# Kernel optimization log

Measured on AMD Instinct MI355X. Metric: run time of the kernel, lower is better.

Reference implementation:

```python
import jax, jax.numpy as jnp
import numpy as np

N = 50000   # nodes
E = 800000  # edges
D = 128     # input = hidden = output dim
G = 64      # graphs in batch


def setup_inputs() -> dict:
    key = jax.random.key(0)
    ks = jax.random.split(key, 12)
    s = 1.0 / np.sqrt(D)
    x = jax.random.normal(ks[0], (N, D), dtype=jnp.float32)
    edge_index = jax.random.randint(ks[1], (2, E), 0, N, dtype=jnp.int64)
    batch = jnp.sort(jax.random.randint(ks[2], (N,), 0, G, dtype=jnp.int64))
    return {
        "x": x,
        "W1": jax.random.normal(ks[3], (D, D), jnp.float32) * s,
        "b1": jnp.zeros((D,), jnp.float32),
        "W2": jax.random.normal(ks[4], (D, D), jnp.float32) * s,
        "b2": jnp.zeros((D,), jnp.float32),
        "W3": jax.random.normal(ks[5], (D, D), jnp.float32) * s,
        "b3": jnp.zeros((D,), jnp.float32),
        "Wm1": jax.random.normal(ks[6], (D, D), jnp.float32) * s,
        "bm1": jnp.zeros((D,), jnp.float32),
        "Wm2": jax.random.normal(ks[7], (D, D), jnp.float32) * s,
        "bm2": jnp.zeros((D,), jnp.float32),
        "edge_index": edge_index,
        "batch": batch,
    }


def _gcn_conv(x, W, b, src, dst, deg_isqrt, num_nodes):
    # PyG GCNConv: h = D^{-1/2}(A+I)D^{-1/2} X W + b  (self-loops included in src/dst)
    h = x @ W  # [N, Dout]
    norm = deg_isqrt[src] * deg_isqrt[dst]  # [E+N]
    msg = h[src] * norm[:, None]            # gather + scale
    out = jax.ops.segment_sum(msg, dst, num_segments=num_nodes)  # scatter-add
    return out + b


def reference(x, W1, b1, W2, b2, W3, b3, Wm1, bm1, Wm2, bm2, edge_index, batch):
    num_nodes = x.shape[0]
    loop = jnp.arange(num_nodes, dtype=edge_index.dtype)
    src = jnp.concatenate([edge_index[0], loop])  # add self-loops
    dst = jnp.concatenate([edge_index[1], loop])
    # degree with self-loops (edge_weight = 1), computed on target nodes
    deg = jax.ops.segment_sum(jnp.ones_like(dst, dtype=x.dtype), dst,
                              num_segments=num_nodes)
    deg_isqrt = jnp.where(deg > 0, jax.lax.rsqrt(deg), 0.0)

    h = jax.nn.relu(_gcn_conv(x, W1, b1, src, dst, deg_isqrt, num_nodes))
    h = jax.nn.relu(_gcn_conv(h, W2, b2, src, dst, deg_isqrt, num_nodes))
    h = _gcn_conv(h, W3, b3, src, dst, deg_isqrt, num_nodes)

    # global_mean_pool over graph ids
    sums = jax.ops.segment_sum(h, batch, num_segments=G)
    cnts = jax.ops.segment_sum(jnp.ones((num_nodes,), h.dtype), batch,
                               num_segments=G)
    pooled = sums / jnp.maximum(cnts, 1.0)[:, None]  # [G, D]

    out = jax.nn.relu(pooled @ Wm1 + bm1) @ Wm2 + bm2
    return out
```

## Files before the change

kernel.cpp:

```cpp
#include <hip/hip_runtime.h>
#include <hip/hip_bf16.h>

typedef __attribute__((ext_vector_type(8))) short short8;
typedef __attribute__((ext_vector_type(4))) float floatx4;

#define SLAB_CAP 96

static __device__ __forceinline__ ushort f2b(float f) {
    __hip_bfloat16 h = __float2bfloat16(f);
    return __builtin_bit_cast(ushort, h);
}
static __device__ __forceinline__ float blo(uint u) {
    return __builtin_bit_cast(float, u << 16);
}
static __device__ __forceinline__ float bhi(uint u) {
    return __builtin_bit_cast(float, u & 0xffff0000u);
}
static __device__ __forceinline__ float b2f(ushort u) {
    return __builtin_bit_cast(float, (uint)u << 16);
}
static __device__ __forceinline__ uint pack2(float lo, float hi) {
    return (uint)f2b(lo) | ((uint)f2b(hi) << 16);
}

static __device__ __forceinline__ void fill_body(int bid, const int* __restrict__ src,
                                                 const int* __restrict__ dst, int E,
                                                 int* __restrict__ deg_cnt,
                                                 int* __restrict__ slab) {
    int e0 = (bid * 256 + threadIdx.x) * 4;
    if (e0 + 3 < E) {
        int4 s = *(const int4*)(src + e0);
        int4 d = *(const int4*)(dst + e0);
        int p0 = atomicAdd(&deg_cnt[d.x], 1);
        int p1 = atomicAdd(&deg_cnt[d.y], 1);
        int p2 = atomicAdd(&deg_cnt[d.z], 1);
        int p3 = atomicAdd(&deg_cnt[d.w], 1);
        if (p0 < SLAB_CAP) slab[d.x * SLAB_CAP + p0] = s.x;
        if (p1 < SLAB_CAP) slab[d.y * SLAB_CAP + p1] = s.y;
        if (p2 < SLAB_CAP) slab[d.z * SLAB_CAP + p2] = s.z;
        if (p3 < SLAB_CAP) slab[d.w * SLAB_CAP + p3] = s.w;
    } else {
        for (int e = e0; e < E; ++e) {
            int d = dst[e];
            int p = atomicAdd(&deg_cnt[d], 1);
            if (p < SLAB_CAP) slab[d * SLAB_CAP + p] = src[e];
        }
    }
}

template <typename XT, int SCALE>
static __device__ __forceinline__ void mm_body(ushort* __restrict__ wt,
                                               const XT* __restrict__ X,
                                               const float* __restrict__ W,
                                               const float* __restrict__ di,
                                               ushort* __restrict__ Y,
                                               int N, int tiles, int tile0, int tstride) {
    int t = threadIdx.x;
    {
        int c0 = (t & 31) * 4;
        int k0 = (t >> 5) * 4;
#pragma unroll
        for (int i = 0; i < 4; i++) {
            int kk = k0 + i * 32;
            float4 r0 = *(const float4*)&W[(kk + 0) * 128 + c0];
            float4 r1 = *(const float4*)&W[(kk + 1) * 128 + c0];
            float4 r2 = *(const float4*)&W[(kk + 2) * 128 + c0];
            float4 r3 = *(const float4*)&W[(kk + 3) * 128 + c0];
            float colv[4][4] = {{r0.x, r1.x, r2.x, r3.x},
                                {r0.y, r1.y, r2.y, r3.y},
                                {r0.z, r1.z, r2.z, r3.z},
                                {r0.w, r1.w, r2.w, r3.w}};
#pragma unroll
            for (int j = 0; j < 4; j++) {
                int c = c0 + j;
                int chs = (kk >> 3) ^ (c & 7);
                int idx = c * 128 + (chs << 3) + (kk & 7);
                ushort4 v;
                v.x = f2b(colv[j][0]); v.y = f2b(colv[j][1]);
                v.z = f2b(colv[j][2]); v.w = f2b(colv[j][3]);
                *(ushort4*)&wt[idx] = v;
            }
        }
    }
    __syncthreads();
    int wv = t >> 6;
    int l  = t & 63;
    int lr = l & 15;
    int lk = l >> 4;
    for (int tile = tile0; tile < tiles; tile += tstride) {
        int row = tile * 64 + wv * 16 + lr;
        int rowc = row < N ? row : N - 1;
        short8 a[4];
#pragma unroll
        for (int ks = 0; ks < 4; ks++) {
            int kb = lk * 8 + ks * 32;
            if constexpr (sizeof(XT) == 4) {
                const float* p = (const float*)X + (size_t)rowc * 128 + kb;
                float4 f0 = *(const float4*)p;
                float4 f1 = *(const float4*)(p + 4);
                short8 av;
                av[0] = (short)f2b(f0.x); av[1] = (short)f2b(f0.y);
                av[2] = (short)f2b(f0.z); av[3] = (short)f2b(f0.w);
                av[4] = (short)f2b(f1.x); av[5] = (short)f2b(f1.y);
                av[6] = (short)f2b(f1.z); av[7] = (short)f2b(f1.w);
                a[ks] = av;
            } else {
                a[ks] = *(const short8*)((const ushort*)X + (size_t)rowc * 128 + kb);
            }
        }
        floatx4 acc[8];
#pragma unroll
        for (int ct = 0; ct < 8; ct++) acc[ct] = (floatx4)(0.f);
#pragma unroll
        for (int ct = 0; ct < 8; ct++) {
            int col = ct * 16 + lr;
#pragma unroll
            for (int ks = 0; ks < 4; ks++) {
                int kb = lk * 8 + ks * 32;
                int chs = (kb >> 3) ^ (col & 7);
                short8 b = *(const short8*)&wt[col * 128 + (chs << 3)];
                acc[ct] = __builtin_amdgcn_mfma_f32_16x16x32_bf16(a[ks], b, acc[ct], 0, 0, 0);
            }
        }
        int rbase = tile * 64 + wv * 16 + lk * 4;
        float dr[4] = {1.f, 1.f, 1.f, 1.f};
        if constexpr (SCALE) {
            if (rbase + 3 < N) {
                float4 d4 = *(const float4*)&di[rbase];
                dr[0] = d4.x; dr[1] = d4.y; dr[2] = d4.z; dr[3] = d4.w;
            } else {
                dr[0] = rbase + 0 < N ? di[rbase + 0] : 0.f;
                dr[1] = rbase + 1 < N ? di[rbase + 1] : 0.f;
                dr[2] = rbase + 2 < N ? di[rbase + 2] : 0.f;
                dr[3] = rbase + 3 < N ? di[rbase + 3] : 0.f;
            }
        }
#pragma unroll
        for (int ct = 0; ct < 8; ct++) {
#pragma unroll
            for (int r = 0; r < 4; r++) {
                int ro = rbase + r;
                if (ro < N) Y[(size_t)ro * 128 + ct * 16 + lr] = f2b(acc[ct][r] * dr[r]);
            }
        }
    }
}

__global__ __launch_bounds__(256) void k_fill_mm(const int* __restrict__ src,
                                                 const int* __restrict__ dst, int E,
                                                 int* __restrict__ deg_cnt,
                                                 int* __restrict__ slab,
                                                 const float* __restrict__ X,
                                                 const float* __restrict__ W,
                                                 ushort* __restrict__ Y,
                                                 int N, int tiles, int fillBlocks) {
    __shared__ ushort wt[128 * 128];
    int bid = blockIdx.x;
    if (bid < fillBlocks) {
        fill_body(bid, src, dst, E, deg_cnt, slab);
        return;
    }
    mm_body<float, 0>(wt, X, W, nullptr, Y, N, tiles, bid - fillBlocks, gridDim.x - fillBlocks);
}

template <typename XT, int SCALE>
__global__ __launch_bounds__(256) void k_matmul_mfma(const XT* __restrict__ X,
                                                     const float* __restrict__ W,
                                                     const float* __restrict__ di,
                                                     ushort* __restrict__ Y,
                                                     int N, int tiles) {
    __shared__ ushort wt[128 * 128];
    mm_body<XT, SCALE>(wt, X, W, di, Y, N, tiles, blockIdx.x, gridDim.x);
}

__global__ __launch_bounds__(256) void k_di_scale(const int* __restrict__ deg_cnt,
                                                  const uint* __restrict__ Hin,
                                                  uint* __restrict__ Hout,
                                                  float* __restrict__ di, int N) {
    int idx = blockIdx.x * 256 + threadIdx.x;
    int n = idx >> 6;
    int l = idx & 63;
    if (n >= N) return;
    float din = rsqrtf((float)(deg_cnt[n] + 1));
    if (l == 0) di[n] = din;
    uint u = Hin[(size_t)n * 64 + l];
    Hout[(size_t)n * 64 + l] = pack2(blo(u) * din, bhi(u) * din);
}

template <int RELU>
__global__ __launch_bounds__(256) void k_aggregate(const uint* __restrict__ H,
                                                   const float* __restrict__ di,
                                                   const int* __restrict__ deg_cnt,
                                                   const int* __restrict__ slab,
                                                   const float* __restrict__ bias,
                                                   uint* __restrict__ Y, int N) {
    int t = threadIdx.x;
    int node = blockIdx.x * 4 + (t >> 6);
    if (node >= N) return;
    int lane = t & 63;
    float din = di[node];
    uint hv = H[(size_t)node * 64 + lane];
    float ax = blo(hv), ay = bhi(hv);
    float bx = 0.f, by = 0.f;
    int deg = deg_cnt[node];
    if (deg > SLAB_CAP) deg = SLAB_CAP;
    const int* row = slab + (size_t)node * SLAB_CAP;
    int e = 0;
    for (; e + 7 < deg; e += 8) {
        int4 i0 = *(const int4*)(row + e);
        int4 i1 = *(const int4*)(row + e + 4);
        uint g0 = H[(size_t)i0.x * 64 + lane];
        uint g1 = H[(size_t)i0.y * 64 + lane];
        uint g2 = H[(size_t)i0.z * 64 + lane];
        uint g3 = H[(size_t)i0.w * 64 + lane];
        uint g4 = H[(size_t)i1.x * 64 + lane];
        uint g5 = H[(size_t)i1.y * 64 + lane];
        uint g6 = H[(size_t)i1.z * 64 + lane];
        uint g7 = H[(size_t)i1.w * 64 + lane];
        ax += blo(g0) + blo(g1) + blo(g2) + blo(g3);
        ay += bhi(g0) + bhi(g1) + bhi(g2) + bhi(g3);
        bx += blo(g4) + blo(g5) + blo(g6) + blo(g7);
        by += bhi(g4) + bhi(g5) + bhi(g6) + bhi(g7);
    }
    for (; e + 3 < deg; e += 4) {
        int4 i0 = *(const int4*)(row + e);
        uint g0 = H[(size_t)i0.x * 64 + lane];
        uint g1 = H[(size_t)i0.y * 64 + lane];
        uint g2 = H[(size_t)i0.z * 64 + lane];
        uint g3 = H[(size_t)i0.w * 64 + lane];
        ax += blo(g0) + blo(g1) + blo(g2) + blo(g3);
        ay += bhi(g0) + bhi(g1) + bhi(g2) + bhi(g3);
    }
    for (; e < deg; ++e) {
        uint g = H[(size_t)row[e] * 64 + lane];
        ax += blo(g); ay += bhi(g);
    }
    ax += bx; ay += by;
    float2 b = *(const float2*)&bias[lane * 2];
    ax = ax * din + b.x; ay = ay * din + b.y;
    if (RELU) { ax = fmaxf(ax, 0.f); ay = fmaxf(ay, 0.f); }
    Y[(size_t)node * 64 + lane] = pack2(ax, ay);
}

__global__ __launch_bounds__(128) void k_pool(const ushort* __restrict__ H,
                                              const int* __restrict__ batch,
                                              float* __restrict__ sums, int N) {
    int d = threadIdx.x;
    int n0 = blockIdx.x * 64;
    int n1 = n0 + 64; if (n1 > N) n1 = N;
    if (n0 >= N) return;
    float acc = 0.f;
    int g = batch[n0];
    for (int n = n0; n < n1; ++n) {
        int gn = batch[n];
        if (gn != g) { atomicAdd(&sums[g * 128 + d], acc); acc = 0.f; g = gn; }
        acc += b2f(H[(size_t)n * 128 + d]);
    }
    atomicAdd(&sums[g * 128 + d], acc);
}

__global__ __launch_bounds__(128) void k_mlp(const float* __restrict__ sums,
                                             const int* __restrict__ batch, int N,
                                             const float* __restrict__ Wm1,
                                             const float* __restrict__ bm1,
                                             const float* __restrict__ Wm2,
                                             const float* __restrict__ bm2,
                                             float* __restrict__ out) {
    __shared__ float p[128], t1[128];
    int g = blockIdx.x, j = threadIdx.x;
    int n0, n1;
    {
        int lo = 0, hi = N;
        while (lo < hi) { int m = (lo + hi) >> 1; if (batch[m] < g) lo = m + 1; else hi = m; }
        n0 = lo;
        hi = N;
        while (lo < hi) { int m = (lo + hi) >> 1; if (batch[m] < g + 1) lo = m + 1; else hi = m; }
        n1 = lo;
    }
    float cnt = (float)(n1 - n0);
    p[j] = sums[g * 128 + j] / fmaxf(cnt, 1.0f);
    __syncthreads();
    float acc = bm1[j];
#pragma unroll 4
    for (int k = 0; k < 128; k++) acc += p[k] * Wm1[k * 128 + j];
    t1[j] = fmaxf(acc, 0.f);
    __syncthreads();
    float acc2 = bm2[j];
#pragma unroll 4
    for (int k = 0; k < 128; k++) acc2 += t1[k] * Wm2[k * 128 + j];
    out[g * 128 + j] = acc2;
}

extern "C" void kernel_launch(void* const* d_in, const int* in_sizes, int n_in,
                              void* d_out, int out_size, void* d_ws, size_t ws_size,
                              hipStream_t stream) {
    const float* x   = (const float*)d_in[0];
    const float* W1  = (const float*)d_in[1];
    const float* b1  = (const float*)d_in[2];
    const float* W2  = (const float*)d_in[3];
    const float* b2  = (const float*)d_in[4];
    const float* W3  = (const float*)d_in[5];
    const float* b3  = (const float*)d_in[6];
    const float* Wm1 = (const float*)d_in[7];
    const float* bm1 = (const float*)d_in[8];
    const float* Wm2 = (const float*)d_in[9];
    const float* bm2 = (const float*)d_in[10];
    const int* edge  = (const int*)d_in[11];
    const int* batch = (const int*)d_in[12];

    int N = in_sizes[0] / 128;
    int E = in_sizes[11] / 2;
    int G = out_size / 128;
    const int* esrc = edge;
    const int* edst = edge + E;

    char* w = (char*)d_ws;
    auto alloc = [&](size_t bytes) -> char* {
        char* p = w;
        w += (bytes + 255) & ~size_t(255);
        return p;
    };
    ushort* Hb     = (ushort*)alloc((size_t)N * 128 * 2);
    ushort* Gb     = (ushort*)alloc((size_t)N * 128 * 2);
    float*  di     = (float*)alloc((size_t)N * 4);
    int*    slab   = (int*)alloc((size_t)N * SLAB_CAP * 4);
    char*  zbase   = w;
    int*   deg_cnt = (int*)alloc((size_t)N * 4);
    float* psums   = (float*)alloc((size_t)G * 128 * 4);
    size_t zbytes  = (size_t)(w - zbase);

    hipMemsetAsync(zbase, 0, zbytes, stream);

    int tiles64 = (N + 63) / 64;
    int mmgrid = tiles64 < 512 ? tiles64 : 512;
    int fillBlocks = (E + 1023) / 1024;

    k_fill_mm<<<fillBlocks + mmgrid, 256, 0, stream>>>(esrc, edst, E, deg_cnt, slab,
                                                       x, W1, Gb, N, tiles64, fillBlocks);
    k_di_scale<<<(N * 64 + 255) / 256, 256, 0, stream>>>(deg_cnt, (const uint*)Gb, (uint*)Hb, di, N);
    k_aggregate<1><<<(N + 3) / 4, 256, 0, stream>>>((const uint*)Hb, di, deg_cnt, slab, b1, (uint*)Gb, N);
    k_matmul_mfma<ushort, 1><<<mmgrid, 256, 0, stream>>>(Gb, W2, di, Hb, N, tiles64);
    k_aggregate<1><<<(N + 3) / 4, 256, 0, stream>>>((const uint*)Hb, di, deg_cnt, slab, b2, (uint*)Gb, N);
    k_matmul_mfma<ushort, 1><<<mmgrid, 256, 0, stream>>>(Gb, W3, di, Hb, N, tiles64);
    k_aggregate<0><<<(N + 3) / 4, 256, 0, stream>>>((const uint*)Hb, di, deg_cnt, slab, b3, (uint*)Gb, N);

    k_pool<<<(N + 63) / 64, 128, 0, stream>>>(Gb, batch, psums, N);
    k_mlp<<<G, 128, 0, stream>>>(psums, batch, N, Wm1, bm1, Wm2, bm2, (float*)d_out);
}
```

Baseline: 324.6 us.

## Fuse degree scaling into aggregate and matmul, fuse pooling into last aggregate

Removes the separate di_scale kernel and the di array. Degree normalization is now computed on the fly from deg_cnt: per-neighbor rsqrt weights in the first aggregate and row scaling in the matmul epilogue. The final aggregate writes straight into per-graph pooled sums, using a shared-memory partial sum when a block's four nodes share one graph, which drops the k_pool kernel and an N×128 write and read. Matmul grids now launch one block per tile instead of capping at 512. In exchange the first aggregate does an extra random deg_cnt gather per edge, and the pooled sums take more global atomics.

```diff
diff --git a/kernel.cpp b/kernel.cpp
--- a/kernel.cpp
+++ b/kernel.cpp
@@ -15,9 +15,6 @@
 }
 static __device__ __forceinline__ float bhi(uint u) {
     return __builtin_bit_cast(float, u & 0xffff0000u);
-}
-static __device__ __forceinline__ float b2f(ushort u) {
-    return __builtin_bit_cast(float, (uint)u << 16);
 }
 static __device__ __forceinline__ uint pack2(float lo, float hi) {
     return (uint)f2b(lo) | ((uint)f2b(hi) << 16);
@@ -52,7 +49,7 @@
 static __device__ __forceinline__ void mm_body(ushort* __restrict__ wt,
                                                const XT* __restrict__ X,
                                                const float* __restrict__ W,
-                                               const float* __restrict__ di,
+                                               const int* __restrict__ degp,
                                                ushort* __restrict__ Y,
                                                int N, int tiles, int tile0, int tstride) {
     int t = threadIdx.x;
@@ -126,13 +123,13 @@
         float dr[4] = {1.f, 1.f, 1.f, 1.f};
         if constexpr (SCALE) {
             if (rbase + 3 < N) {
-                float4 d4 = *(const float4*)&di[rbase];
-                dr[0] = d4.x; dr[1] = d4.y; dr[2] = d4.z; dr[3] = d4.w;
+                int4 d4 = *(const int4*)&degp[rbase];
+                dr[0] = rsqrtf((float)(d4.x + 1)); dr[1] = rsqrtf((float)(d4.y + 1));
+                dr[2] = rsqrtf((float)(d4.z + 1)); dr[3] = rsqrtf((float)(d4.w + 1));
             } else {
-                dr[0] = rbase + 0 < N ? di[rbase + 0] : 0.f;
-                dr[1] = rbase + 1 < N ? di[rbase + 1] : 0.f;
-                dr[2] = rbase + 2 < N ? di[rbase + 2] : 0.f;
-                dr[3] = rbase + 3 < N ? di[rbase + 3] : 0.f;
+#pragma unroll
+                for (int r = 0; r < 4; r++)
+                    dr[r] = rbase + r < N ? rsqrtf((float)(degp[rbase + r] + 1)) : 0.f;
             }
         }
 #pragma unroll
@@ -166,97 +163,118 @@
 template <typename XT, int SCALE>
 __global__ __launch_bounds__(256) void k_matmul_mfma(const XT* __restrict__ X,
                                                      const float* __restrict__ W,
-                                                     const float* __restrict__ di,
+                                                     const int* __restrict__ degp,
                                                      ushort* __restrict__ Y,
                                                      int N, int tiles) {
     __shared__ ushort wt[128 * 128];
-    mm_body<XT, SCALE>(wt, X, W, di, Y, N, tiles, blockIdx.x, gridDim.x);
-}
-
-__global__ __launch_bounds__(256) void k_di_scale(const int* __restrict__ deg_cnt,
-                                                  const uint* __restrict__ Hin,
-                                                  uint* __restrict__ Hout,
-                                                  float* __restrict__ di, int N) {
-    int idx = blockIdx.x * 256 + threadIdx.x;
-    int n = idx >> 6;
-    int l = idx & 63;
-    if (n >= N) return;
-    float din = rsqrtf((float)(deg_cnt[n] + 1));
-    if (l == 0) di[n] = din;
-    uint u = Hin[(size_t)n * 64 + l];
-    Hout[(size_t)n * 64 + l] = pack2(blo(u) * din, bhi(u) * din);
-}
-
-template <int RELU>
+    mm_body<XT, SCALE>(wt, X, W, degp, Y, N, tiles, blockIdx.x, gridDim.x);
+}
+
+template <int MODE>
 __global__ __launch_bounds__(256) void k_aggregate(const uint* __restrict__ H,
-                                                   const float* __restrict__ di,
                                                    const int* __restrict__ deg_cnt,
                                                    const int* __restrict__ slab,
                                                    const float* __restrict__ bias,
-                                                   uint* __restrict__ Y, int N) {
+                                                   uint* __restrict__ Y,
+                                                   const int* __restrict__ batch,
+                                                   float* __restrict__ psums, int N) {
     int t = threadIdx.x;
     int node = blockIdx.x * 4 + (t >> 6);
-    if (node >= N) return;
     int lane = t & 63;
-    float din = di[node];
-    uint hv = H[(size_t)node * 64 + lane];
-    float ax = blo(hv), ay = bhi(hv);
-    float bx = 0.f, by = 0.f;
-    int deg = deg_cnt[node];
-    if (deg > SLAB_CAP) deg = SLAB_CAP;
-    const int* row = slab + (size_t)node * SLAB_CAP;
-    int e = 0;
-    for (; e + 7 < deg; e += 8) {
-        int4 i0 = *(const int4*)(row + e);
-        int4 i1 = *(const int4*)(row + e + 4);
-        uint g0 = H[(size_t)i0.x * 64 + lane];
-        uint g1 = H[(size_t)i0.y * 64 + lane];
-        uint g2 = H[(size_t)i0.z * 64 + lane];
-        uint g3 = H[(size_t)i0.w * 64 + lane];
-        uint g4 = H[(size_t)i1.x * 64 + lane];
-        uint g5 = H[(size_t)i1.y * 64 + lane];
-        uint g6 = H[(size_t)i1.z * 64 + lane];
-        uint g7 = H[(size_t)i1.w * 64 + lane];
-        ax += blo(g0) + blo(g1) + blo(g2) + blo(g3);
-        ay += bhi(g0) + bhi(g1) + bhi(g2) + bhi(g3);
-        bx += blo(g4) + blo(g5) + blo(g6) + blo(g7);
-        by += bhi(g4) + bhi(g5) + bhi(g6) + bhi(g7);
-    }
-    for (; e + 3 < deg; e += 4) {
-        int4 i0 = *(const int4*)(row + e);
-        uint g0 = H[(size_t)i0.x * 64 + lane];
-        uint g1 = H[(size_t)i0.y * 64 + lane];
-        uint g2 = H[(size_t)i0.z * 64 + lane];
-        uint g3 = H[(size_t)i0.w * 64 + lane];
-        ax += blo(g0) + blo(g1) + blo(g2) + blo(g3);
-        ay += bhi(g0) + bhi(g1) + bhi(g2) + bhi(g3);
-    }
-    for (; e < deg; ++e) {
-        uint g = H[(size_t)row[e] * 64 + lane];
-        ax += blo(g); ay += bhi(g);
-    }
-    ax += bx; ay += by;
-    float2 b = *(const float2*)&bias[lane * 2];
-    ax = ax * din + b.x; ay = ay * din + b.y;
-    if (RELU) { ax = fmaxf(ax, 0.f); ay = fmaxf(ay, 0.f); }
-    Y[(size_t)node * 64 + lane] = pack2(ax, ay);
-}
-
-__global__ __launch_bounds__(128) void k_pool(const ushort* __restrict__ H,
-                                              const int* __restrict__ batch,
-                                              float* __restrict__ sums, int N) {
-    int d = threadIdx.x;
-    int n0 = blockIdx.x * 64;
-    int n1 = n0 + 64; if (n1 > N) n1 = N;
-    if (n0 >= N) return;
-    float acc = 0.f;
-    int g = batch[n0];
-    for (int n = n0; n < n1; ++n) {
-        int gn = batch[n];
-        if (gn != g) { atomicAdd(&sums[g * 128 + d], acc); acc = 0.f; g = gn; }
-        acc += b2f(H[(size_t)n * 128 + d]);
-    }
-    atomicAdd(&sums[g * 128 + d], acc);
+    bool valid = node < N;
+    float ax = 0.f, ay = 0.f;
+    if (valid) {
+        int degn = deg_cnt[node];
+        float din = rsqrtf((float)(degn + 1));
+        uint hv = H[(size_t)node * 64 + lane];
+        if constexpr (MODE == 0) { ax = din * blo(hv); ay = din * bhi(hv); }
+        else { ax = blo(hv); ay = bhi(hv); }
+        int deg = degn > SLAB_CAP ? SLAB_CAP : degn;
+        const int* row = slab + (size_t)node * SLAB_CAP;
+        int e = 0;
+        if constexpr (MODE == 0) {
+            for (; e + 3 < deg; e += 4) {
+                int4 i0 = *(const int4*)(row + e);
+                int d0 = deg_cnt[i0.x], d1 = deg_cnt[i0.y];
+                int d2 = deg_cnt[i0.z], d3 = deg_cnt[i0.w];
+                uint g0 = H[(size_t)i0.x * 64 + lane];
+                uint g1 = H[(size_t)i0.y * 64 + lane];
+                uint g2 = H[(size_t)i0.z * 64 + lane];
+                uint g3 = H[(size_t)i0.w * 64 + lane];
+                float w0 = rsqrtf((float)(d0 + 1)), w1 = rsqrtf((float)(d1 + 1));
+                float w2 = rsqrtf((float)(d2 + 1)), w3 = rsqrtf((float)(d3 + 1));
+                ax += blo(g0) * w0 + blo(g1) * w1 + blo(g2) * w2 + blo(g3) * w3;
+                ay += bhi(g0) * w0 + bhi(g1) * w1 + bhi(g2) * w2 + bhi(g3) * w3;
+            }
+            for (; e < deg; ++e) {
+                int s = row[e];
+                float ws = rsqrtf((float)(deg_cnt[s] + 1));
+                uint g = H[(size_t)s * 64 + lane];
+                ax += blo(g) * ws; ay += bhi(g) * ws;
+            }
+        } else {
+            float bx = 0.f, by = 0.f;
+            for (; e + 7 < deg; e += 8) {
+                int4 i0 = *(const int4*)(row + e);
+                int4 i1 = *(const int4*)(row + e + 4);
+                uint g0 = H[(size_t)i0.x * 64 + lane];
+                uint g1 = H[(size_t)i0.y * 64 + lane];
+                uint g2 = H[(size_t)i0.z * 64 + lane];
+                uint g3 = H[(size_t)i0.w * 64 + lane];
+                uint g4 = H[(size_t)i1.x * 64 + lane];
+                uint g5 = H[(size_t)i1.y * 64 + lane];
+                uint g6 = H[(size_t)i1.z * 64 + lane];
+                uint g7 = H[(size_t)i1.w * 64 + lane];
+                ax += blo(g0) + blo(g1) + blo(g2) + blo(g3);
+                ay += bhi(g0) + bhi(g1) + bhi(g2) + bhi(g3);
+                bx += blo(g4) + blo(g5) + blo(g6) + blo(g7);
+                by += bhi(g4) + bhi(g5) + bhi(g6) + bhi(g7);
+            }
+            for (; e + 3 < deg; e += 4) {
+                int4 i0 = *(const int4*)(row + e);
+                uint g0 = H[(size_t)i0.x * 64 + lane];
+                uint g1 = H[(size_t)i0.y * 64 + lane];
+                uint g2 = H[(size_t)i0.z * 64 + lane];
+                uint g3 = H[(size_t)i0.w * 64 + lane];
+                ax += blo(g0) + blo(g1) + blo(g2) + blo(g3);
+                ay += bhi(g0) + bhi(g1) + bhi(g2) + bhi(g3);
+            }
+            for (; e < deg; ++e) {
+                uint g = H[(size_t)row[e] * 64 + lane];
+                ax += blo(g); ay += bhi(g);
+            }
+            ax += bx; ay += by;
+        }
+        float2 b = *(const float2*)&bias[lane * 2];
+        ax = ax * din + b.x; ay = ay * din + b.y;
+        if constexpr (MODE != 2) {
+            ax = fmaxf(ax, 0.f); ay = fmaxf(ay, 0.f);
+            Y[(size_t)node * 64 + lane] = pack2(ax, ay);
+        }
+    }
+    if constexpr (MODE == 2) {
+        __shared__ float ls[128];
+        if (t < 128) ls[t] = 0.f;
+        __syncthreads();
+        int nbase = blockIdx.x * 4;
+        if (nbase >= N) return;
+        int nlast = nbase + 3 < N ? nbase + 3 : N - 1;
+        int gf = batch[nbase], gl = batch[nlast];
+        if (gf == gl) {
+            if (valid) {
+                atomicAdd(&ls[lane * 2], ax);
+                atomicAdd(&ls[lane * 2 + 1], ay);
+            }
+            __syncthreads();
+            if (t < 128) atomicAdd(&psums[gf * 128 + t], ls[t]);
+        } else {
+            if (valid) {
+                int g = batch[node];
+                atomicAdd(&psums[g * 128 + lane * 2], ax);
+                atomicAdd(&psums[g * 128 + lane * 2 + 1], ay);
+            }
+        }
+    }
 }
 
 __global__ __launch_bounds__(128) void k_mlp(const float* __restrict__ sums,
@@ -322,7 +340,6 @@
     };
     ushort* Hb     = (ushort*)alloc((size_t)N * 128 * 2);
     ushort* Gb     = (ushort*)alloc((size_t)N * 128 * 2);
-    float*  di     = (float*)alloc((size_t)N * 4);
     int*    slab   = (int*)alloc((size_t)N * SLAB_CAP * 4);
     char*  zbase   = w;
     int*   deg_cnt = (int*)alloc((size_t)N * 4);
@@ -332,18 +349,18 @@
     hipMemsetAsync(zbase, 0, zbytes, stream);
 
     int tiles64 = (N + 63) / 64;
-    int mmgrid = tiles64 < 512 ? tiles64 : 512;
     int fillBlocks = (E + 1023) / 1024;
 
-    k_fill_mm<<<fillBlocks + mmgrid, 256, 0, stream>>>(esrc, edst, E, deg_cnt, slab,
-                                                       x, W1, Gb, N, tiles64, fillBlocks);
-    k_di_scale<<<(N * 64 + 255) / 256, 256, 0, stream>>>(deg_cnt, (const uint*)Gb, (uint*)Hb, di, N);
-    k_aggregate<1><<<(N + 3) / 4, 256, 0, stream>>>((const uint*)Hb, di, deg_cnt, slab, b1, (uint*)Gb, N);
-    k_matmul_mfma<ushort, 1><<<mmgrid, 256, 0, stream>>>(Gb, W2, di, Hb, N, tiles64);
-    k_aggregate<1><<<(N + 3) / 4, 256, 0, stream>>>((const uint*)Hb, di, deg_cnt, slab, b2, (uint*)Gb, N);
-    k_matmul_mfma<ushort, 1><<<mmgrid, 256, 0, stream>>>(Gb, W3, di, Hb, N, tiles64);
-    k_aggregate<0><<<(N + 3) / 4, 256, 0, stream>>>((const uint*)Hb, di, deg_cnt, slab, b3, (uint*)Gb, N);
-
-    k_pool<<<(N + 63) / 64, 128, 0, stream>>>(Gb, batch, psums, N);
+    k_fill_mm<<<fillBlocks + tiles64, 256, 0, stream>>>(esrc, edst, E, deg_cnt, slab,
+                                                        x, W1, Gb, N, tiles64, fillBlocks);
+    k_aggregate<0><<<(N + 3) / 4, 256, 0, stream>>>((const uint*)Gb, deg_cnt, slab, b1,
+                                                    (uint*)Hb, nullptr, nullptr, N);
+    k_matmul_mfma<ushort, 1><<<tiles64, 256, 0, stream>>>(Hb, W2, deg_cnt, Gb, N, tiles64);
+    k_aggregate<1><<<(N + 3) / 4, 256, 0, stream>>>((const uint*)Gb, deg_cnt, slab, b2,
+                                                    (uint*)Hb, nullptr, nullptr, N);
+    k_matmul_mfma<ushort, 1><<<tiles64, 256, 0, stream>>>(Hb, W3, deg_cnt, Gb, N, tiles64);
+    k_aggregate<2><<<(N + 3) / 4, 256, 0, stream>>>((const uint*)Gb, deg_cnt, slab, b3,
+                                                    nullptr, batch, psums, N);
+
     k_mlp<<<G, 128, 0, stream>>>(psums, batch, N, Wm1, bm1, Wm2, bm2, (float*)d_out);
 }
```

Result: no change. 324.9 us (+0.1%).
